# Kernel tuning notes

Measured on AMD Instinct MI355X. Metric: run time of the kernel, lower is better.

Reference implementation:

```python
import math
import jax, jax.numpy as jnp
import numpy as np
from jax import lax

B = 32; SEQ_LEN = 1024; PRED_LEN = 1024; ENC_IN = 7; MARK = 4; C_OUT = 7
D_MODEL = 128; D_INNER = 256; D_STATE = 16; D_CONV = 4; DT_RANK = 8; N_LAYER = 2


def setup_inputs() -> dict:
    key = jax.random.key(0)
    ks = jax.random.split(key, 16)
    f32 = jnp.float32
    inp = {}
    inp['x_enc'] = jax.random.normal(ks[0], (B, SEQ_LEN, ENC_IN), f32)
    inp['x_mark_enc'] = jax.random.uniform(ks[1], (B, SEQ_LEN, MARK), f32) - 0.5
    inp['x_dec'] = jax.random.normal(ks[2], (B, 512, ENC_IN), f32)
    inp['x_mark_dec'] = jax.random.uniform(ks[3], (B, 512, MARK), f32) - 0.5
    inp['token_W'] = jax.random.normal(ks[4], (D_MODEL, ENC_IN, 3), f32) * (1.0 / math.sqrt(3 * ENC_IN))
    inp['temporal_W'] = jax.random.normal(ks[5], (D_MODEL, MARK), f32) * 0.1
    inp['norm_w'] = jnp.ones((N_LAYER, D_MODEL), f32)
    inp['norm_b'] = jnp.zeros((N_LAYER, D_MODEL), f32)
    inp['in_proj_W'] = jax.random.normal(ks[6], (N_LAYER, 2 * D_INNER, D_MODEL), f32) * (1.0 / math.sqrt(D_MODEL))
    inp['conv_W'] = jax.random.normal(ks[7], (N_LAYER, D_INNER, D_CONV), f32) * 0.3
    inp['conv_b'] = jnp.zeros((N_LAYER, D_INNER), f32)
    inp['x_proj_W'] = jax.random.normal(ks[8], (N_LAYER, DT_RANK + 2 * D_STATE, D_INNER), f32) * (1.0 / math.sqrt(D_INNER))
    inp['dt_proj_W'] = jax.random.normal(ks[9], (N_LAYER, D_INNER, DT_RANK), f32) * (1.0 / math.sqrt(DT_RANK))
    inp['dt_proj_b'] = jax.random.normal(ks[10], (N_LAYER, D_INNER), f32) * 0.5 - 4.0  # softplus -> small dt, like mamba init
    inp['A_log'] = jnp.log(jnp.broadcast_to(jnp.arange(1, D_STATE + 1, dtype=f32), (N_LAYER, D_INNER, D_STATE)))
    inp['D_param'] = jnp.ones((N_LAYER, D_INNER), f32)
    inp['out_proj_W'] = jax.random.normal(ks[11], (N_LAYER, D_MODEL, D_INNER), f32) * (1.0 / math.sqrt(D_INNER))
    inp['normf_w'] = jnp.ones((D_MODEL,), f32)
    inp['normf_b'] = jnp.zeros((D_MODEL,), f32)
    inp['out_W'] = jax.random.normal(ks[12], (C_OUT, D_MODEL), f32) * (1.0 / math.sqrt(D_MODEL))
    return inp


def _layer_norm(x, w, b):
    mu = x.mean(-1, keepdims=True)
    var = ((x - mu) ** 2).mean(-1, keepdims=True)
    return (x - mu) * lax.rsqrt(var + 1e-5) * w + b


def _silu(x):
    return x * jax.nn.sigmoid(x)


def _pos_embedding(L, d):
    pos = jnp.arange(L, dtype=jnp.float32)[:, None]
    div = jnp.exp(jnp.arange(0, d, 2, dtype=jnp.float32) * (-math.log(10000.0) / d))
    pe = jnp.zeros((L, d), jnp.float32)
    pe = pe.at[:, 0::2].set(jnp.sin(pos * div))
    pe = pe.at[:, 1::2].set(jnp.cos(pos * div))
    return pe


def _embed(x_enc, x_mark_enc, token_W, temporal_W):
    # TokenEmbedding: Conv1d(enc_in->d_model, k=3, circular padding, no bias)
    xp = jnp.concatenate([x_enc[:, -1:], x_enc, x_enc[:, :1]], axis=1)  # circular pad by 1
    val = lax.conv_general_dilated(xp, token_W.transpose(2, 1, 0), (1,), 'VALID',
                                   dimension_numbers=('NWC', 'WIO', 'NWC'))
    temp = jnp.einsum('blf,df->bld', x_mark_enc, temporal_W)  # TimeFeatureEmbedding (no bias)
    return val + temp + _pos_embedding(x_enc.shape[1], D_MODEL)


def _mamba_mixer(x, in_W, cW, cb, xp_W, dtW, dtb, A_log_l, D_l, o_W):
    Bb, L, _ = x.shape
    xz = jnp.einsum('bld,ed->ble', x, in_W)  # [B,L,2*d_inner]
    xi, z = jnp.split(xz, 2, axis=-1)
    # causal depthwise conv1d (kernel d_conv)
    xpad = jnp.pad(xi, ((0, 0), (D_CONV - 1, 0), (0, 0)))
    kern = cW.T[:, None, :]  # [d_conv, 1, d_inner]
    u = lax.conv_general_dilated(xpad, kern, (1,), 'VALID', dimension_numbers=('NWC', 'WIO', 'NWC'),
                                 feature_group_count=D_INNER) + cb
    u = _silu(u)
    dbc = jnp.einsum('bld,ed->ble', u, xp_W)
    dt_r = dbc[..., :DT_RANK]
    Bm = dbc[..., DT_RANK:DT_RANK + D_STATE]
    Cm = dbc[..., DT_RANK + D_STATE:]
    dt = jax.nn.softplus(jnp.einsum('blr,dr->bld', dt_r, dtW) + dtb)  # [B,L,d_inner]
    A = -jnp.exp(A_log_l)  # [d_inner, d_state]

    def step(h, inp):
        dt_t, B_t, C_t, u_t = inp  # [B,d_inner], [B,d_state], [B,d_state], [B,d_inner]
        dA = jnp.exp(dt_t[..., None] * A)
        h = dA * h + dt_t[..., None] * B_t[:, None, :] * u_t[..., None]
        y = jnp.einsum('bds,bs->bd', h, C_t)
        return h, y

    h0 = jnp.zeros((Bb, D_INNER, D_STATE), x.dtype)
    _, ys = lax.scan(step, h0, (dt.transpose(1, 0, 2), Bm.transpose(1, 0, 2),
                                Cm.transpose(1, 0, 2), u.transpose(1, 0, 2)))
    y = ys.transpose(1, 0, 2) + u * D_l  # skip connection D*u
    y = y * _silu(z)
    return jnp.einsum('ble,de->bld', y, o_W)


def _mixer_model(x, norm_w, norm_b, in_proj_W, conv_W, conv_b, x_proj_W, dt_proj_W, dt_proj_b,
                 A_log, D_param, out_proj_W, normf_w, normf_b):
    hidden, residual = x, None
    for l in range(N_LAYER):
        residual = hidden if residual is None else hidden + residual
        hidden = _mamba_mixer(_layer_norm(residual, norm_w[l], norm_b[l]), in_proj_W[l], conv_W[l],
                              conv_b[l], x_proj_W[l], dt_proj_W[l], dt_proj_b[l], A_log[l],
                              D_param[l], out_proj_W[l])
    return _layer_norm(hidden + residual, normf_w, normf_b)


def reference(x_enc, x_mark_enc, x_dec, x_mark_dec, token_W, temporal_W, norm_w, norm_b,
              in_proj_W, conv_W, conv_b, x_proj_W, dt_proj_W, dt_proj_b, A_log, D_param,
              out_proj_W, normf_w, normf_b, out_W):
    h = _embed(x_enc, x_mark_enc, token_W, temporal_W)
    outs = []
    for _ in range((PRED_LEN - 1) // SEQ_LEN + 1):
        h = _mixer_model(h, norm_w, norm_b, in_proj_W, conv_W, conv_b, x_proj_W, dt_proj_W,
                         dt_proj_b, A_log, D_param, out_proj_W, normf_w, normf_b)
        outs.append(h)
    mamba_out = jnp.concatenate(outs, axis=1)[:, :PRED_LEN]
    return jnp.einsum('bld,cd->blc', mamba_out, out_W)
```

## Files before the change

### kernel.cpp

```cpp
#include <hip/hip_runtime.h>
#include <math.h>

#define B_  32
#define L_  1024
#define M_  (B_*L_)
#define DM  128
#define DI  256
#define DS  16
#define DC  4
#define DR  8
#define NL  2

__device__ __forceinline__ float silu_f(float x) { return x / (1.f + expf(-x)); }
__device__ __forceinline__ float softplus_f(float x) {
    return fmaxf(x, 0.f) + log1pf(expf(-fabsf(x)));
}

__global__ __launch_bounds__(256) void pe_kernel(float* __restrict__ pe) {
    int idx = blockIdx.x * 256 + threadIdx.x;
    int t = idx >> 6, i = idx & 63;
    float div = expf(-0.07195578415606394f * (float)(2 * i));
    float ang = (float)t * div;
    pe[t * 128 + 2 * i]     = sinf(ang);
    pe[t * 128 + 2 * i + 1] = cosf(ang);
}

__global__ __launch_bounds__(256) void embed_kernel(
        const float* __restrict__ x_enc, const float* __restrict__ x_mark,
        const float* __restrict__ tokW, const float* __restrict__ tempW,
        const float* __restrict__ pe, float* __restrict__ out) {
    int idx = blockIdx.x * 256 + threadIdx.x;
    int d = idx & 127;
    int m = idx >> 7;
    int b = m >> 10, t = m & 1023;
    const float* xb = x_enc + (size_t)b * L_ * 7;
    float acc = pe[t * 128 + d];
    #pragma unroll
    for (int w = 0; w < 3; ++w) {
        int tt = t + w - 1;
        tt = (tt < 0) ? (L_ - 1) : (tt >= L_ ? 0 : tt);
        const float* xr = xb + tt * 7;
        #pragma unroll
        for (int f = 0; f < 7; ++f) acc += xr[f] * tokW[(d * 7 + f) * 3 + w];
    }
    const float* mr = x_mark + (size_t)m * 4;
    #pragma unroll
    for (int f = 0; f < 4; ++f) acc += mr[f] * tempW[d * 4 + f];
    out[idx] = acc;
}

__global__ __launch_bounds__(256) void ln_kernel(
        const float* __restrict__ a, const float* __restrict__ b,
        const float* __restrict__ w, const float* __restrict__ bias,
        float* __restrict__ out_ln, float* __restrict__ out_res) {
    int wv = threadIdx.x >> 6, lane = threadIdx.x & 63;
    size_t m = (size_t)blockIdx.x * 4 + wv;
    size_t base = m * DM;
    float x0 = a[base + lane], x1 = a[base + lane + 64];
    if (b) { x0 += b[base + lane]; x1 += b[base + lane + 64]; }
    if (out_res) { out_res[base + lane] = x0; out_res[base + lane + 64] = x1; }
    float s = x0 + x1;
    #pragma unroll
    for (int o = 1; o < 64; o <<= 1) s += __shfl_xor(s, o, 64);
    float mu = s * (1.f / 128.f);
    float d0 = x0 - mu, d1 = x1 - mu;
    float v = d0 * d0 + d1 * d1;
    #pragma unroll
    for (int o = 1; o < 64; o <<= 1) v += __shfl_xor(v, o, 64);
    float inv = rsqrtf(v * (1.f / 128.f) + 1e-5f);
    out_ln[base + lane]      = d0 * inv * w[lane]      + bias[lane];
    out_ln[base + lane + 64] = d1 * inv * w[lane + 64] + bias[lane + 64];
}

__global__ __launch_bounds__(256) void gemm_inproj(
        const float* __restrict__ A, const float* __restrict__ W,
        float* __restrict__ xiT, float* __restrict__ zsilT) {
    __shared__ float As[32][128];
    __shared__ float Ws[32][128];
    int bm = blockIdx.y * 128, bn = blockIdx.x * 128;
    int tid = threadIdx.x, tx = tid & 15, ty = tid >> 4;
    float acc[8][8] = {};
    for (int k0 = 0; k0 < 128; k0 += 32) {
        #pragma unroll
        for (int i = 0; i < 4; ++i) {
            int idx = i * 256 + tid;
            int row = idx >> 3, c4 = (idx & 7) * 4;
            float4 a4 = *(const float4*)(A + (size_t)(bm + row) * 128 + k0 + c4);
            As[c4 + 0][row] = a4.x; As[c4 + 1][row] = a4.y;
            As[c4 + 2][row] = a4.z; As[c4 + 3][row] = a4.w;
            float4 w4 = *(const float4*)(W + (size_t)(bn + row) * 128 + k0 + c4);
            Ws[c4 + 0][row] = w4.x; Ws[c4 + 1][row] = w4.y;
            Ws[c4 + 2][row] = w4.z; Ws[c4 + 3][row] = w4.w;
        }
        __syncthreads();
        #pragma unroll
        for (int k = 0; k < 32; ++k) {
            float a[8], bb[8];
            *(float4*)&a[0]  = *(float4*)&As[k][ty * 8];
            *(float4*)&a[4]  = *(float4*)&As[k][ty * 8 + 4];
            *(float4*)&bb[0] = *(float4*)&Ws[k][tx * 8];
            *(float4*)&bb[4] = *(float4*)&Ws[k][tx * 8 + 4];
            #pragma unroll
            for (int i = 0; i < 8; ++i)
                #pragma unroll
                for (int j = 0; j < 8; ++j) acc[i][j] += a[i] * bb[j];
        }
        __syncthreads();
    }
    int b = bm >> 10, t0 = (bm & 1023) + ty * 8;
    if (bn < 256) {
        #pragma unroll
        for (int j = 0; j < 8; ++j) {
            int xd = bn + tx * 8 + j;
            float r[8];
            #pragma unroll
            for (int i = 0; i < 8; ++i) r[i] = acc[i][j];
            float* dst = xiT + ((size_t)(b * 256 + xd)) * 1024 + t0;
            *(float4*)dst       = *(float4*)&r[0];
            *(float4*)(dst + 4) = *(float4*)&r[4];
        }
    } else {
        #pragma unroll
        for (int j = 0; j < 8; ++j) {
            int zd = bn - 256 + tx * 8 + j;
            float r[8];
            #pragma unroll
            for (int i = 0; i < 8; ++i) r[i] = silu_f(acc[i][j]);
            float* dst = zsilT + ((size_t)(b * 256 + zd)) * 1024 + t0;
            *(float4*)dst       = *(float4*)&r[0];
            *(float4*)(dst + 4) = *(float4*)&r[4];
        }
    }
}

__global__ __launch_bounds__(256) void gemm_tn_128(
        const float* __restrict__ AT, const float* __restrict__ W,
        float* __restrict__ C, int M, int N, int K) {
    __shared__ float As[32][128];
    __shared__ float Ws[32][128];
    int bm = blockIdx.y * 128, bn = blockIdx.x * 128;
    int b = bm >> 10, tloc = bm & 1023;
    int tid = threadIdx.x, tx = tid & 15, ty = tid >> 4;
    float acc[8][8] = {};
    for (int k0 = 0; k0 < K; k0 += 32) {
        #pragma unroll
        for (int i = 0; i < 4; ++i) {
            int idx = i * 256 + tid;
            int k = idx >> 5, m4 = (idx & 31) * 4;
            float4 a4 = *(const float4*)(AT + ((size_t)b * K + k0 + k) * 1024 + tloc + m4);
            *(float4*)&As[k][m4] = a4;
            int row = idx >> 3, c4 = (idx & 7) * 4;
            float4 w4 = *(const float4*)(W + (size_t)(bn + row) * K + k0 + c4);
            Ws[c4 + 0][row] = w4.x; Ws[c4 + 1][row] = w4.y;
            Ws[c4 + 2][row] = w4.z; Ws[c4 + 3][row] = w4.w;
        }
        __syncthreads();
        #pragma unroll
        for (int k = 0; k < 32; ++k) {
            float a[8], bb[8];
            *(float4*)&a[0]  = *(float4*)&As[k][ty * 8];
            *(float4*)&a[4]  = *(float4*)&As[k][ty * 8 + 4];
            *(float4*)&bb[0] = *(float4*)&Ws[k][tx * 8];
            *(float4*)&bb[4] = *(float4*)&Ws[k][tx * 8 + 4];
            #pragma unroll
            for (int i = 0; i < 8; ++i)
                #pragma unroll
                for (int j = 0; j < 8; ++j) acc[i][j] += a[i] * bb[j];
        }
        __syncthreads();
    }
    #pragma unroll
    for (int i = 0; i < 8; ++i) {
        size_t row = (size_t)(bm + ty * 8 + i) * N + bn + tx * 8;
        *(float4*)(C + row)     = *(float4*)&acc[i][0];
        *(float4*)(C + row + 4) = *(float4*)&acc[i][4];
    }
}

__global__ __launch_bounds__(256) void gemm_tn_64(
        const float* __restrict__ AT, const float* __restrict__ W,
        float* __restrict__ C, int M, int N, int K) {
    __shared__ float As[16][68];
    __shared__ float Ws[16][68];
    int bm = blockIdx.y * 64, bn = blockIdx.x * 64;
    int b = bm >> 10, tloc = bm & 1023;
    int tid = threadIdx.x, tx = tid & 15, ty = tid >> 4;
    float acc[4][4] = {};
    for (int k0 = 0; k0 < K; k0 += 16) {
        {
            int k = tid >> 4, m4 = (tid & 15) * 4;
            float4 a4 = *(const float4*)(AT + ((size_t)b * K + k0 + k) * 1024 + tloc + m4);
            *(float4*)&As[k][m4] = a4;
        }
        #pragma unroll
        for (int i = 0; i < 4; ++i) {
            int r = i * 16 + ty;
            int n = bn + r;
            Ws[tx][r] = (n < N) ? W[(size_t)n * K + k0 + tx] : 0.f;
        }
        __syncthreads();
        #pragma unroll
        for (int k = 0; k < 16; ++k) {
            float a[4], bb[4];
            #pragma unroll
            for (int i = 0; i < 4; ++i) a[i] = As[k][ty * 4 + i];
            #pragma unroll
            for (int j = 0; j < 4; ++j) bb[j] = Ws[k][tx * 4 + j];
            #pragma unroll
            for (int i = 0; i < 4; ++i)
                #pragma unroll
                for (int j = 0; j < 4; ++j) acc[i][j] += a[i] * bb[j];
        }
        __syncthreads();
    }
    #pragma unroll
    for (int i = 0; i < 4; ++i) {
        int m = bm + ty * 4 + i;
        #pragma unroll
        for (int j = 0; j < 4; ++j) {
            int n = bn + tx * 4 + j;
            if (n < N) C[(size_t)m * N + n] = acc[i][j];
        }
    }
}

__global__ __launch_bounds__(256) void conv_T_kernel(
        const float* __restrict__ xiT, const float* __restrict__ cw,
        const float* __restrict__ cb, float* __restrict__ uT) {
    int wv = threadIdx.x >> 6, lane = threadIdx.x & 63;
    int rid = blockIdx.x * 4 + wv;
    int d = rid & 255;
    const float* src = xiT + (size_t)rid * 1024;
    int t0 = lane * 16;
    float x[20];
    {
        float4 p = (lane > 0) ? *(const float4*)(src + t0 - 4)
                              : make_float4(0.f, 0.f, 0.f, 0.f);
        *(float4*)&x[0] = p;
        #pragma unroll
        for (int c = 0; c < 4; ++c)
            *(float4*)&x[4 + c * 4] = *(const float4*)(src + t0 + c * 4);
    }
    float4 w4 = ((const float4*)cw)[d];
    float bias = cb[d];
    float* dst = uT + (size_t)rid * 1024 + t0;
    #pragma unroll
    for (int c = 0; c < 4; ++c) {
        float r[4];
        #pragma unroll
        for (int i = 0; i < 4; ++i) {
            int k = c * 4 + i;
            float acc = bias + x[k + 1] * w4.x + x[k + 2] * w4.y
                             + x[k + 3] * w4.z + x[k + 4] * w4.w;
            r[i] = silu_f(acc);
        }
        *(float4*)(dst + c * 4) = make_float4(r[0], r[1], r[2], r[3]);
    }
}

__global__ __launch_bounds__(256) void dbc_split_kernel(
        const float* __restrict__ dbc, const float* __restrict__ dtW,
        const float* __restrict__ dtb, float* __restrict__ dtT,
        float* __restrict__ BT, float* __restrict__ CT) {
    int m0 = blockIdx.x * 64;
    int b = m0 >> 10, t0 = m0 & 1023;
    {
        int n = threadIdx.x;
        float4 wa = ((const float4*)dtW)[n * 2];
        float4 wb = ((const float4*)dtW)[n * 2 + 1];
        float bias = dtb[n];
        float* dst = dtT + ((size_t)(b * 256 + n)) * 1024 + t0;
        for (int r4 = 0; r4 < 64; r4 += 4) {
            float o[4];
            #pragma unroll
            for (int i = 0; i < 4; ++i) {
                const float* row = dbc + (size_t)(m0 + r4 + i) * 40;
                float acc = bias + row[0] * wa.x + row[1] * wa.y + row[2] * wa.z + row[3] * wa.w
                                 + row[4] * wb.x + row[5] * wb.y + row[6] * wb.z + row[7] * wb.w;
                o[i] = softplus_f(acc);
            }
            *(float4*)(dst + r4) = make_float4(o[0], o[1], o[2], o[3]);
        }
    }
    {
        int s = threadIdx.x >> 3, q = threadIdx.x & 7;
        const float* src = dbc + (size_t)m0 * 40 + 8 + s;
        float* outp = ((s < 16) ? BT : CT) + ((size_t)(b * 16 + (s & 15))) * 1024 + t0 + q * 8;
        float v[8];
        #pragma unroll
        for (int i = 0; i < 8; ++i) v[i] = src[(size_t)(q * 8 + i) * 40];
        *(float4*)outp       = make_float4(v[0], v[1], v[2], v[3]);
        *(float4*)(outp + 4) = make_float4(v[4], v[5], v[6], v[7]);
    }
}

__global__ __launch_bounds__(256) void scan5_kernel(
        const float* __restrict__ dtT, const float* __restrict__ uT,
        const float* __restrict__ BT, const float* __restrict__ CT,
        const float* __restrict__ A_log, const float* __restrict__ zsilT,
        const float* __restrict__ Dp, float* __restrict__ yT) {
    int wv = threadIdx.x >> 6, lane = threadIdx.x & 63;
    int wid = blockIdx.x * 4 + wv;
    int b = wid >> 8, d = wid & 255;
    size_t base = (size_t)wid * 1024 + lane * 16;

    float dt[16], du[16], y[16], pcA[16], pcB[16];
    {
        const float4* p = (const float4*)(dtT + base);
        const float4* q = (const float4*)(uT + base);
        #pragma unroll
        for (int c = 0; c < 4; ++c) {
            float4 dv = p[c], uv = q[c];
            dt[c * 4 + 0] = dv.x; dt[c * 4 + 1] = dv.y; dt[c * 4 + 2] = dv.z; dt[c * 4 + 3] = dv.w;
            du[c * 4 + 0] = dv.x * uv.x; du[c * 4 + 1] = dv.y * uv.y;
            du[c * 4 + 2] = dv.z * uv.z; du[c * 4 + 3] = dv.w * uv.w;
        }
        #pragma unroll
        for (int i = 0; i < 16; ++i) y[i] = 0.f;
    }
    const float* Bb = BT + (size_t)b * 16 * 1024 + lane * 16;
    const float* Cb = CT + (size_t)b * 16 * 1024 + lane * 16;
    const float* Arow = A_log + d * 16;

    for (int p = 0; p < 8; ++p) {
        int s0 = 2 * p, s1 = 2 * p + 1;
        float4 B0[4], B1[4], C0[4], C1[4];
        #pragma unroll
        for (int c = 0; c < 4; ++c) {
            B0[c] = *(const float4*)(Bb + (size_t)s0 * 1024 + c * 4);
            B1[c] = *(const float4*)(Bb + (size_t)s1 * 1024 + c * 4);
            C0[c] = *(const float4*)(Cb + (size_t)s0 * 1024 + c * 4);
            C1[c] = *(const float4*)(Cb + (size_t)s1 * 1024 + c * 4);
        }
        float A2a = -expf(Arow[s0]) * 1.4426950408889634f;
        float A2b = -expf(Arow[s1]) * 1.4426950408889634f;
        float h0 = 0.f, P0 = 1.f, h1 = 0.f, P1 = 1.f;
        #pragma unroll
        for (int c = 0; c < 4; ++c) {
            float Bv0[4] = {B0[c].x, B0[c].y, B0[c].z, B0[c].w};
            float Cv0[4] = {C0[c].x, C0[c].y, C0[c].z, C0[c].w};
            float Bv1[4] = {B1[c].x, B1[c].y, B1[c].z, B1[c].w};
            float Cv1[4] = {C1[c].x, C1[c].y, C1[c].z, C1[c].w};
            #pragma unroll
            for (int i = 0; i < 4; ++i) {
                int ii = c * 4 + i;
                float a0 = __builtin_amdgcn_exp2f(dt[ii] * A2a);
                float a1 = __builtin_amdgcn_exp2f(dt[ii] * A2b);
                h0 = a0 * h0 + du[ii] * Bv0[i];  P0 *= a0;
                h1 = a1 * h1 + du[ii] * Bv1[i];  P1 *= a1;
                y[ii] += h0 * Cv0[i] + h1 * Cv1[i];
                pcA[ii] = P0 * Cv0[i];
                pcB[ii] = P1 * Cv1[i];
            }
        }
        float Aag0 = P0, E0 = h0, Aag1 = P1, E1 = h1;
        #pragma unroll
        for (int dlt = 1; dlt < 64; dlt <<= 1) {
            float Au0 = __shfl_up(Aag0, dlt, 64), Eu0 = __shfl_up(E0, dlt, 64);
            float Au1 = __shfl_up(Aag1, dlt, 64), Eu1 = __shfl_up(E1, dlt, 64);
            if (lane >= dlt) {
                E0 = Aag0 * Eu0 + E0;  Aag0 *= Au0;
                E1 = Aag1 * Eu1 + E1;  Aag1 *= Au1;
            }
        }
        float car0 = __shfl_up(E0, 1, 64), car1 = __shfl_up(E1, 1, 64);
        if (lane == 0) { car0 = 0.f; car1 = 0.f; }
        #pragma unroll
        for (int i = 0; i < 16; ++i) y[i] += car0 * pcA[i] + car1 * pcB[i];
    }

    float Dv = Dp[d];
    const float4* qz = (const float4*)(zsilT + base);
    float* dst = yT + base;
    #pragma unroll
    for (int c = 0; c < 4; ++c) {
        float4 zv = qz[c];
        float za[4] = {zv.x, zv.y, zv.z, zv.w};
        float r[4];
        #pragma unroll
        for (int i = 0; i < 4; ++i) {
            int ii = c * 4 + i;
            float u = (dt[ii] > 0.f) ? du[ii] * __builtin_amdgcn_rcpf(dt[ii]) : 0.f;
            r[i] = (y[ii] + u * Dv) * za[i];
        }
        *(float4*)(dst + c * 4) = make_float4(r[0], r[1], r[2], r[3]);
    }
}

__global__ __launch_bounds__(256) void outproj_kernel(
        const float* __restrict__ x, const float* __restrict__ W,
        float* __restrict__ out) {
    int wv = threadIdx.x >> 6, lane = threadIdx.x & 63;
    size_t m = (size_t)blockIdx.x * 4 + wv;
    float x0 = x[m * 128 + lane], x1 = x[m * 128 + lane + 64];
    #pragma unroll
    for (int c = 0; c < 7; ++c) {
        float p = x0 * W[c * 128 + lane] + x1 * W[c * 128 + lane + 64];
        #pragma unroll
        for (int o = 1; o < 64; o <<= 1) p += __shfl_xor(p, o, 64);
        if (lane == 0) out[m * 7 + c] = p;
    }
}

extern "C" void kernel_launch(void* const* d_in, const int* in_sizes, int n_in,
                              void* d_out, int out_size, void* d_ws, size_t ws_size,
                              hipStream_t stream) {
    const float* x_enc  = (const float*)d_in[0];
    const float* x_mark = (const float*)d_in[1];
    const float* tokW   = (const float*)d_in[4];
    const float* tempW  = (const float*)d_in[5];
    const float* norm_w = (const float*)d_in[6];
    const float* norm_b = (const float*)d_in[7];
    const float* inW    = (const float*)d_in[8];
    const float* convW  = (const float*)d_in[9];
    const float* convB  = (const float*)d_in[10];
    const float* xpW    = (const float*)d_in[11];
    const float* dtW    = (const float*)d_in[12];
    const float* dtbp   = (const float*)d_in[13];
    const float* A_log  = (const float*)d_in[14];
    const float* Dp     = (const float*)d_in[15];
    const float* outW   = (const float*)d_in[16];
    const float* nfw    = (const float*)d_in[17];
    const float* nfb    = (const float*)d_in[18];
    const float* finW   = (const float*)d_in[19];
    float* out = (float*)d_out;

    float* ws = (float*)d_ws;
    size_t o = 0;
    float* hidden   = ws + o; o += (size_t)M_ * DM;
    float* residual = ws + o; o += (size_t)M_ * DM;
    float* xln      = ws + o; o += (size_t)M_ * DM;
    float* xiT      = ws + o; o += (size_t)M_ * DI;
    float* zsilT    = ws + o; o += (size_t)M_ * DI;
    float* uT       = ws + o; o += (size_t)M_ * DI;
    float* dbc      = ws + o; o += (size_t)M_ * 40;
    float* dtT      = ws + o; o += (size_t)M_ * DI;
    float* yT       = ws + o; o += (size_t)M_ * DI;
    float* BT = xln;
    float* CT = xln + (size_t)B_ * DS * L_;
    float* pe = dbc;

    dim3 blk(256);
    pe_kernel<<<1024 * 64 / 256, blk, 0, stream>>>(pe);
    embed_kernel<<<M_ * DM / 256, blk, 0, stream>>>(x_enc, x_mark, tokW, tempW, pe, hidden);

    for (int l = 0; l < NL; ++l) {
        ln_kernel<<<M_ / 4, blk, 0, stream>>>(hidden, l ? residual : nullptr,
                                              norm_w + l * DM, norm_b + l * DM,
                                              xln, residual);
        gemm_inproj<<<dim3(4, M_ / 128), blk, 0, stream>>>(
            xln, inW + (size_t)l * 512 * DM, xiT, zsilT);
        conv_T_kernel<<<B_ * DI / 4, blk, 0, stream>>>(xiT, convW + l * DI * DC,
                                                       convB + l * DI, uT);
        gemm_tn_64<<<dim3(1, M_ / 64), blk, 0, stream>>>(
            uT, xpW + (size_t)l * 40 * DI, dbc, M_, 40, DI);
        dbc_split_kernel<<<M_ / 64, blk, 0, stream>>>(dbc, dtW + l * DI * DR,
                                                      dtbp + l * DI, dtT, BT, CT);
        scan5_kernel<<<B_ * DI / 4, blk, 0, stream>>>(dtT, uT, BT, CT,
                                                      A_log + l * DI * DS, zsilT,
                                                      Dp + l * DI, yT);
        gemm_tn_128<<<dim3(1, M_ / 128), blk, 0, stream>>>(
            yT, outW + (size_t)l * DM * DI, hidden, M_, DM, DI);
    }

    ln_kernel<<<M_ / 4, blk, 0, stream>>>(hidden, residual, nfw, nfb, xln, nullptr);
    outproj_kernel<<<M_ / 4, blk, 0, stream>>>(xln, finW, out);
}
```

Measured before the change: 696.5 us.

## Move projection GEMMs to split-bf16 MFMA with packed hi/lo activations

Replaces the three FP32 SIMT GEMMs (in_proj, x_proj, out_proj) with MFMA bf16 kernels that use a three-term hi/lo split (hi*hi + hi*lo + lo*hi) to keep roughly FP32 accuracy. The producers (layernorm, conv, scan) now emit activations as packed bf16 hi/lo pairs, and weights are converted once per call. The x_proj output is stored transposed so the separate dt/B/C split kernel becomes a smaller dt-only kernel, and scan reads B and C directly from it. This trades three MFMAs per tile, extra conversion work and some precision loss for tensor-core throughput on the GEMMs.

```diff
diff --git a/kernel.cpp b/kernel.cpp
--- a/kernel.cpp
+++ b/kernel.cpp
@@ -11,9 +11,38 @@
 #define DR  8
 #define NL  2
 
+typedef unsigned int  uint32;
+typedef unsigned short ush;
+typedef __attribute__((ext_vector_type(8))) short bf16x8;
+typedef __attribute__((ext_vector_type(4))) float f32x4;
+
 __device__ __forceinline__ float silu_f(float x) { return x / (1.f + expf(-x)); }
 __device__ __forceinline__ float softplus_f(float x) {
     return fmaxf(x, 0.f) + log1pf(expf(-fabsf(x)));
+}
+__device__ __forceinline__ ush f2bf(float x) {
+    union { float f; uint32 u; } v; v.f = x;
+    uint32 lsb = (v.u >> 16) & 1u;
+    v.u += 0x7fffu + lsb;
+    return (ush)(v.u >> 16);
+}
+__device__ __forceinline__ void split2(float x, ush& h, ush& l) {
+    h = f2bf(x);
+    float fh = __uint_as_float(((uint32)h) << 16);
+    l = f2bf(x - fh);
+}
+__device__ __forceinline__ uint32 pack_pair(float x) {
+    ush h, l; split2(x, h, l);
+    return (uint32)h | ((uint32)l << 16);
+}
+__device__ __forceinline__ float unpack_pair(uint32 v) {
+    return __uint_as_float(v << 16) + __uint_as_float(v & 0xffff0000u);
+}
+
+__global__ __launch_bounds__(256) void cvt_pair_kernel(
+        const float* __restrict__ src, ush* __restrict__ h, ush* __restrict__ l, int n) {
+    int i = blockIdx.x * 256 + threadIdx.x;
+    if (i < n) { ush hh, ll; split2(src[i], hh, ll); h[i] = hh; l[i] = ll; }
 }
 
 __global__ __launch_bounds__(256) void pe_kernel(float* __restrict__ pe) {
@@ -52,7 +81,8 @@
 __global__ __launch_bounds__(256) void ln_kernel(
         const float* __restrict__ a, const float* __restrict__ b,
         const float* __restrict__ w, const float* __restrict__ bias,
-        float* __restrict__ out_ln, float* __restrict__ out_res) {
+        float* __restrict__ out_f32, ush* __restrict__ outh, ush* __restrict__ outl,
+        float* __restrict__ out_res) {
     int wv = threadIdx.x >> 6, lane = threadIdx.x & 63;
     size_t m = (size_t)blockIdx.x * 4 + wv;
     size_t base = m * DM;
@@ -68,165 +98,162 @@
     #pragma unroll
     for (int o = 1; o < 64; o <<= 1) v += __shfl_xor(v, o, 64);
     float inv = rsqrtf(v * (1.f / 128.f) + 1e-5f);
-    out_ln[base + lane]      = d0 * inv * w[lane]      + bias[lane];
-    out_ln[base + lane + 64] = d1 * inv * w[lane + 64] + bias[lane + 64];
-}
-
-__global__ __launch_bounds__(256) void gemm_inproj(
-        const float* __restrict__ A, const float* __restrict__ W,
+    float r0 = d0 * inv * w[lane]      + bias[lane];
+    float r1 = d1 * inv * w[lane + 64] + bias[lane + 64];
+    if (out_f32) {
+        out_f32[base + lane] = r0; out_f32[base + lane + 64] = r1;
+    } else {
+        ush h, l;
+        split2(r0, h, l); outh[base + lane] = h;      outl[base + lane] = l;
+        split2(r1, h, l); outh[base + lane + 64] = h; outl[base + lane + 64] = l;
+    }
+}
+
+__global__ __launch_bounds__(256) void gemm_inproj_mfma(
+        const ush* __restrict__ Ah, const ush* __restrict__ Al,
+        const ush* __restrict__ Wh, const ush* __restrict__ Wl,
         float* __restrict__ xiT, float* __restrict__ zsilT) {
-    __shared__ float As[32][128];
-    __shared__ float Ws[32][128];
     int bm = blockIdx.y * 128, bn = blockIdx.x * 128;
-    int tid = threadIdx.x, tx = tid & 15, ty = tid >> 4;
-    float acc[8][8] = {};
+    int w = threadIdx.x >> 6, l = threadIdx.x & 63;
+    int lm = l & 15, lk8 = (l >> 4) * 8;
+    f32x4 acc[2][8];
+    #pragma unroll
+    for (int mi = 0; mi < 2; ++mi)
+        #pragma unroll
+        for (int ni = 0; ni < 8; ++ni) acc[mi][ni] = {0.f, 0.f, 0.f, 0.f};
+    const ush* ah = Ah + (size_t)(bm + w * 32 + lm) * 128;
+    const ush* al = Al + (size_t)(bm + w * 32 + lm) * 128;
+    const ush* wh = Wh + (size_t)(bn + lm) * 128;
+    const ush* wl = Wl + (size_t)(bn + lm) * 128;
     for (int k0 = 0; k0 < 128; k0 += 32) {
-        #pragma unroll
-        for (int i = 0; i < 4; ++i) {
-            int idx = i * 256 + tid;
-            int row = idx >> 3, c4 = (idx & 7) * 4;
-            float4 a4 = *(const float4*)(A + (size_t)(bm + row) * 128 + k0 + c4);
-            As[c4 + 0][row] = a4.x; As[c4 + 1][row] = a4.y;
-            As[c4 + 2][row] = a4.z; As[c4 + 3][row] = a4.w;
-            float4 w4 = *(const float4*)(W + (size_t)(bn + row) * 128 + k0 + c4);
-            Ws[c4 + 0][row] = w4.x; Ws[c4 + 1][row] = w4.y;
-            Ws[c4 + 2][row] = w4.z; Ws[c4 + 3][row] = w4.w;
-        }
+        bf16x8 aH[2], aL[2];
+        #pragma unroll
+        for (int mi = 0; mi < 2; ++mi) {
+            aH[mi] = *(const bf16x8*)(ah + mi * 16 * 128 + k0 + lk8);
+            aL[mi] = *(const bf16x8*)(al + mi * 16 * 128 + k0 + lk8);
+        }
+        #pragma unroll
+        for (int ni = 0; ni < 8; ++ni) {
+            bf16x8 wH = *(const bf16x8*)(wh + ni * 16 * 128 + k0 + lk8);
+            bf16x8 wLo = *(const bf16x8*)(wl + ni * 16 * 128 + k0 + lk8);
+            #pragma unroll
+            for (int mi = 0; mi < 2; ++mi) {
+                acc[mi][ni] = __builtin_amdgcn_mfma_f32_16x16x32_bf16(aL[mi], wH,  acc[mi][ni], 0, 0, 0);
+                acc[mi][ni] = __builtin_amdgcn_mfma_f32_16x16x32_bf16(aH[mi], wLo, acc[mi][ni], 0, 0, 0);
+                acc[mi][ni] = __builtin_amdgcn_mfma_f32_16x16x32_bf16(aH[mi], wH,  acc[mi][ni], 0, 0, 0);
+            }
+        }
+    }
+    int b = bm >> 10;
+    int tl0 = (bm & 1023) + w * 32 + (l >> 4) * 4;
+    #pragma unroll
+    for (int ni = 0; ni < 8; ++ni) {
+        int n = bn + ni * 16 + lm;
+        #pragma unroll
+        for (int mi = 0; mi < 2; ++mi) {
+            int tl = tl0 + mi * 16;
+            f32x4 v = acc[mi][ni];
+            if (bn < 256) {
+                *(f32x4*)(xiT + ((size_t)(b * 256 + n)) * 1024 + tl) = v;
+            } else {
+                f32x4 r;
+                #pragma unroll
+                for (int i = 0; i < 4; ++i) r[i] = silu_f(v[i]);
+                *(f32x4*)(zsilT + ((size_t)(b * 256 + n - 256)) * 1024 + tl) = r;
+            }
+        }
+    }
+}
+
+template<int NF, int KTOT>
+__global__ __launch_bounds__(256) void gemm_at_mfma(
+        const uint32* __restrict__ A32, const ush* __restrict__ Wh,
+        const ush* __restrict__ Wl, int Nvalid,
+        float* __restrict__ Cnm, float* __restrict__ Cmn) {
+    __shared__ uint32 As[128][68];
+    int bm = blockIdx.x * 128;
+    int b = bm >> 10, tloc = bm & 1023;
+    int tid = threadIdx.x;
+    int w = tid >> 6, l = tid & 63;
+    int lm = l & 15, lk8 = (l >> 4) * 8;
+    f32x4 acc[2][NF];
+    #pragma unroll
+    for (int mi = 0; mi < 2; ++mi)
+        #pragma unroll
+        for (int ni = 0; ni < NF; ++ni) acc[mi][ni] = {0.f, 0.f, 0.f, 0.f};
+
+    for (int k0 = 0; k0 < KTOT; k0 += 64) {
         __syncthreads();
-        #pragma unroll
-        for (int k = 0; k < 32; ++k) {
-            float a[8], bb[8];
-            *(float4*)&a[0]  = *(float4*)&As[k][ty * 8];
-            *(float4*)&a[4]  = *(float4*)&As[k][ty * 8 + 4];
-            *(float4*)&bb[0] = *(float4*)&Ws[k][tx * 8];
-            *(float4*)&bb[4] = *(float4*)&Ws[k][tx * 8 + 4];
+        {
+            int k = tid >> 2, mq = tid & 3;
+            const uint32* src = A32 + ((size_t)(b * KTOT + k0 + k)) * 1024 + tloc + mq * 32;
             #pragma unroll
-            for (int i = 0; i < 8; ++i)
+            for (int c = 0; c < 8; ++c) {
+                uint4 v = *(const uint4*)(src + c * 4);
+                As[mq * 32 + c * 4 + 0][k] = v.x;
+                As[mq * 32 + c * 4 + 1][k] = v.y;
+                As[mq * 32 + c * 4 + 2][k] = v.z;
+                As[mq * 32 + c * 4 + 3][k] = v.w;
+            }
+        }
+        __syncthreads();
+        #pragma unroll
+        for (int ks = 0; ks < 2; ++ks) {
+            int kk = ks * 32 + lk8;
+            bf16x8 aH[2], aL[2];
+            #pragma unroll
+            for (int mi = 0; mi < 2; ++mi) {
+                int m = w * 32 + mi * 16 + lm;
+                uint4 p0 = *(const uint4*)&As[m][kk];
+                uint4 p1 = *(const uint4*)&As[m][kk + 4];
+                uint32 u[8] = {p0.x, p0.y, p0.z, p0.w, p1.x, p1.y, p1.z, p1.w};
+                bf16x8 h, lo;
                 #pragma unroll
-                for (int j = 0; j < 8; ++j) acc[i][j] += a[i] * bb[j];
-        }
-        __syncthreads();
-    }
-    int b = bm >> 10, t0 = (bm & 1023) + ty * 8;
-    if (bn < 256) {
-        #pragma unroll
-        for (int j = 0; j < 8; ++j) {
-            int xd = bn + tx * 8 + j;
-            float r[8];
+                for (int j = 0; j < 8; ++j) {
+                    h[j]  = (short)(u[j] & 0xffffu);
+                    lo[j] = (short)(u[j] >> 16);
+                }
+                aH[mi] = h; aL[mi] = lo;
+            }
             #pragma unroll
-            for (int i = 0; i < 8; ++i) r[i] = acc[i][j];
-            float* dst = xiT + ((size_t)(b * 256 + xd)) * 1024 + t0;
-            *(float4*)dst       = *(float4*)&r[0];
-            *(float4*)(dst + 4) = *(float4*)&r[4];
-        }
-    } else {
-        #pragma unroll
-        for (int j = 0; j < 8; ++j) {
-            int zd = bn - 256 + tx * 8 + j;
-            float r[8];
-            #pragma unroll
-            for (int i = 0; i < 8; ++i) r[i] = silu_f(acc[i][j]);
-            float* dst = zsilT + ((size_t)(b * 256 + zd)) * 1024 + t0;
-            *(float4*)dst       = *(float4*)&r[0];
-            *(float4*)(dst + 4) = *(float4*)&r[4];
-        }
-    }
-}
-
-__global__ __launch_bounds__(256) void gemm_tn_128(
-        const float* __restrict__ AT, const float* __restrict__ W,
-        float* __restrict__ C, int M, int N, int K) {
-    __shared__ float As[32][128];
-    __shared__ float Ws[32][128];
-    int bm = blockIdx.y * 128, bn = blockIdx.x * 128;
-    int b = bm >> 10, tloc = bm & 1023;
-    int tid = threadIdx.x, tx = tid & 15, ty = tid >> 4;
-    float acc[8][8] = {};
-    for (int k0 = 0; k0 < K; k0 += 32) {
-        #pragma unroll
-        for (int i = 0; i < 4; ++i) {
-            int idx = i * 256 + tid;
-            int k = idx >> 5, m4 = (idx & 31) * 4;
-            float4 a4 = *(const float4*)(AT + ((size_t)b * K + k0 + k) * 1024 + tloc + m4);
-            *(float4*)&As[k][m4] = a4;
-            int row = idx >> 3, c4 = (idx & 7) * 4;
-            float4 w4 = *(const float4*)(W + (size_t)(bn + row) * K + k0 + c4);
-            Ws[c4 + 0][row] = w4.x; Ws[c4 + 1][row] = w4.y;
-            Ws[c4 + 2][row] = w4.z; Ws[c4 + 3][row] = w4.w;
-        }
-        __syncthreads();
-        #pragma unroll
-        for (int k = 0; k < 32; ++k) {
-            float a[8], bb[8];
-            *(float4*)&a[0]  = *(float4*)&As[k][ty * 8];
-            *(float4*)&a[4]  = *(float4*)&As[k][ty * 8 + 4];
-            *(float4*)&bb[0] = *(float4*)&Ws[k][tx * 8];
-            *(float4*)&bb[4] = *(float4*)&Ws[k][tx * 8 + 4];
-            #pragma unroll
-            for (int i = 0; i < 8; ++i)
+            for (int ni = 0; ni < NF; ++ni) {
+                int n = ni * 16 + lm;
+                bf16x8 wH = {0,0,0,0,0,0,0,0}, wLo = {0,0,0,0,0,0,0,0};
+                if (n < Nvalid) {
+                    wH  = *(const bf16x8*)(Wh + (size_t)n * KTOT + k0 + ks * 32 + lk8);
+                    wLo = *(const bf16x8*)(Wl + (size_t)n * KTOT + k0 + ks * 32 + lk8);
+                }
                 #pragma unroll
-                for (int j = 0; j < 8; ++j) acc[i][j] += a[i] * bb[j];
-        }
-        __syncthreads();
-    }
-    #pragma unroll
-    for (int i = 0; i < 8; ++i) {
-        size_t row = (size_t)(bm + ty * 8 + i) * N + bn + tx * 8;
-        *(float4*)(C + row)     = *(float4*)&acc[i][0];
-        *(float4*)(C + row + 4) = *(float4*)&acc[i][4];
-    }
-}
-
-__global__ __launch_bounds__(256) void gemm_tn_64(
-        const float* __restrict__ AT, const float* __restrict__ W,
-        float* __restrict__ C, int M, int N, int K) {
-    __shared__ float As[16][68];
-    __shared__ float Ws[16][68];
-    int bm = blockIdx.y * 64, bn = blockIdx.x * 64;
-    int b = bm >> 10, tloc = bm & 1023;
-    int tid = threadIdx.x, tx = tid & 15, ty = tid >> 4;
-    float acc[4][4] = {};
-    for (int k0 = 0; k0 < K; k0 += 16) {
-        {
-            int k = tid >> 4, m4 = (tid & 15) * 4;
-            float4 a4 = *(const float4*)(AT + ((size_t)b * K + k0 + k) * 1024 + tloc + m4);
-            *(float4*)&As[k][m4] = a4;
-        }
-        #pragma unroll
-        for (int i = 0; i < 4; ++i) {
-            int r = i * 16 + ty;
-            int n = bn + r;
-            Ws[tx][r] = (n < N) ? W[(size_t)n * K + k0 + tx] : 0.f;
-        }
-        __syncthreads();
-        #pragma unroll
-        for (int k = 0; k < 16; ++k) {
-            float a[4], bb[4];
-            #pragma unroll
-            for (int i = 0; i < 4; ++i) a[i] = As[k][ty * 4 + i];
-            #pragma unroll
-            for (int j = 0; j < 4; ++j) bb[j] = Ws[k][tx * 4 + j];
-            #pragma unroll
-            for (int i = 0; i < 4; ++i)
+                for (int mi = 0; mi < 2; ++mi) {
+                    acc[mi][ni] = __builtin_amdgcn_mfma_f32_16x16x32_bf16(aL[mi], wH,  acc[mi][ni], 0, 0, 0);
+                    acc[mi][ni] = __builtin_amdgcn_mfma_f32_16x16x32_bf16(aH[mi], wLo, acc[mi][ni], 0, 0, 0);
+                    acc[mi][ni] = __builtin_amdgcn_mfma_f32_16x16x32_bf16(aH[mi], wH,  acc[mi][ni], 0, 0, 0);
+                }
+            }
+        }
+    }
+    int m0 = w * 32 + (l >> 4) * 4;
+    #pragma unroll
+    for (int ni = 0; ni < NF; ++ni) {
+        int n = ni * 16 + lm;
+        #pragma unroll
+        for (int mi = 0; mi < 2; ++mi) {
+            f32x4 v = acc[mi][ni];
+            int mg = bm + m0 + mi * 16;
+            if (Cnm) {
+                if (n < Nvalid) *(f32x4*)(Cnm + (size_t)n * M_ + mg) = v;
+            } else {
                 #pragma unroll
-                for (int j = 0; j < 4; ++j) acc[i][j] += a[i] * bb[j];
-        }
-        __syncthreads();
-    }
-    #pragma unroll
-    for (int i = 0; i < 4; ++i) {
-        int m = bm + ty * 4 + i;
-        #pragma unroll
-        for (int j = 0; j < 4; ++j) {
-            int n = bn + tx * 4 + j;
-            if (n < N) C[(size_t)m * N + n] = acc[i][j];
+                for (int r = 0; r < 4; ++r)
+                    Cmn[(size_t)(mg + r) * Nvalid + n] = v[r];
+            }
         }
     }
 }
 
 __global__ __launch_bounds__(256) void conv_T_kernel(
         const float* __restrict__ xiT, const float* __restrict__ cw,
-        const float* __restrict__ cb, float* __restrict__ uT) {
+        const float* __restrict__ cb, uint32* __restrict__ uT32) {
     int wv = threadIdx.x >> 6, lane = threadIdx.x & 63;
     int rid = blockIdx.x * 4 + wv;
     int d = rid & 255;
@@ -243,62 +270,56 @@
     }
     float4 w4 = ((const float4*)cw)[d];
     float bias = cb[d];
-    float* dst = uT + (size_t)rid * 1024 + t0;
+    uint32* dst = uT32 + (size_t)rid * 1024 + t0;
     #pragma unroll
     for (int c = 0; c < 4; ++c) {
-        float r[4];
+        uint4 o;
+        uint32 ov[4];
         #pragma unroll
         for (int i = 0; i < 4; ++i) {
             int k = c * 4 + i;
             float acc = bias + x[k + 1] * w4.x + x[k + 2] * w4.y
                              + x[k + 3] * w4.z + x[k + 4] * w4.w;
-            r[i] = silu_f(acc);
-        }
-        *(float4*)(dst + c * 4) = make_float4(r[0], r[1], r[2], r[3]);
-    }
-}
-
-__global__ __launch_bounds__(256) void dbc_split_kernel(
-        const float* __restrict__ dbc, const float* __restrict__ dtW,
-        const float* __restrict__ dtb, float* __restrict__ dtT,
-        float* __restrict__ BT, float* __restrict__ CT) {
+            ov[i] = pack_pair(silu_f(acc));
+        }
+        o.x = ov[0]; o.y = ov[1]; o.z = ov[2]; o.w = ov[3];
+        *(uint4*)(dst + c * 4) = o;
+    }
+}
+
+__global__ __launch_bounds__(256) void dtT_kernel(
+        const float* __restrict__ dbcT, const float* __restrict__ dtW,
+        const float* __restrict__ dtb, float* __restrict__ dtT) {
+    int n = threadIdx.x;
     int m0 = blockIdx.x * 64;
     int b = m0 >> 10, t0 = m0 & 1023;
-    {
-        int n = threadIdx.x;
-        float4 wa = ((const float4*)dtW)[n * 2];
-        float4 wb = ((const float4*)dtW)[n * 2 + 1];
-        float bias = dtb[n];
-        float* dst = dtT + ((size_t)(b * 256 + n)) * 1024 + t0;
-        for (int r4 = 0; r4 < 64; r4 += 4) {
-            float o[4];
+    float wk[8];
+    *(float4*)&wk[0] = ((const float4*)dtW)[n * 2];
+    *(float4*)&wk[4] = ((const float4*)dtW)[n * 2 + 1];
+    float bias = dtb[n];
+    float* dst = dtT + ((size_t)(b * 256 + n)) * 1024 + t0;
+    for (int r4 = 0; r4 < 64; r4 += 4) {
+        float col[8][4];
+        #pragma unroll
+        for (int k = 0; k < 8; ++k)
+            *(float4*)col[k] = *(const float4*)(dbcT + (size_t)k * M_ + m0 + r4);
+        float o[4];
+        #pragma unroll
+        for (int i = 0; i < 4; ++i) {
+            float a = bias;
             #pragma unroll
-            for (int i = 0; i < 4; ++i) {
-                const float* row = dbc + (size_t)(m0 + r4 + i) * 40;
-                float acc = bias + row[0] * wa.x + row[1] * wa.y + row[2] * wa.z + row[3] * wa.w
-                                 + row[4] * wb.x + row[5] * wb.y + row[6] * wb.z + row[7] * wb.w;
-                o[i] = softplus_f(acc);
-            }
-            *(float4*)(dst + r4) = make_float4(o[0], o[1], o[2], o[3]);
-        }
-    }
-    {
-        int s = threadIdx.x >> 3, q = threadIdx.x & 7;
-        const float* src = dbc + (size_t)m0 * 40 + 8 + s;
-        float* outp = ((s < 16) ? BT : CT) + ((size_t)(b * 16 + (s & 15))) * 1024 + t0 + q * 8;
-        float v[8];
-        #pragma unroll
-        for (int i = 0; i < 8; ++i) v[i] = src[(size_t)(q * 8 + i) * 40];
-        *(float4*)outp       = make_float4(v[0], v[1], v[2], v[3]);
-        *(float4*)(outp + 4) = make_float4(v[4], v[5], v[6], v[7]);
+            for (int k = 0; k < 8; ++k) a += col[k][i] * wk[k];
+            o[i] = softplus_f(a);
+        }
+        *(float4*)(dst + r4) = make_float4(o[0], o[1], o[2], o[3]);
     }
 }
 
 __global__ __launch_bounds__(256) void scan5_kernel(
-        const float* __restrict__ dtT, const float* __restrict__ uT,
-        const float* __restrict__ BT, const float* __restrict__ CT,
-        const float* __restrict__ A_log, const float* __restrict__ zsilT,
-        const float* __restrict__ Dp, float* __restrict__ yT) {
+        const float* __restrict__ dtT, const uint32* __restrict__ uT32,
+        const float* __restrict__ dbcT, const float* __restrict__ A_log,
+        const float* __restrict__ zsilT, const float* __restrict__ Dp,
+        uint32* __restrict__ yT32) {
     int wv = threadIdx.x >> 6, lane = threadIdx.x & 63;
     int wid = blockIdx.x * 4 + wv;
     int b = wid >> 8, d = wid & 255;
@@ -307,19 +328,21 @@
     float dt[16], du[16], y[16], pcA[16], pcB[16];
     {
         const float4* p = (const float4*)(dtT + base);
-        const float4* q = (const float4*)(uT + base);
+        const uint4*  q = (const uint4*)(uT32 + base);
         #pragma unroll
         for (int c = 0; c < 4; ++c) {
-            float4 dv = p[c], uv = q[c];
+            float4 dv = p[c]; uint4 uv = q[c];
             dt[c * 4 + 0] = dv.x; dt[c * 4 + 1] = dv.y; dt[c * 4 + 2] = dv.z; dt[c * 4 + 3] = dv.w;
-            du[c * 4 + 0] = dv.x * uv.x; du[c * 4 + 1] = dv.y * uv.y;
-            du[c * 4 + 2] = dv.z * uv.z; du[c * 4 + 3] = dv.w * uv.w;
+            du[c * 4 + 0] = dv.x * unpack_pair(uv.x);
+            du[c * 4 + 1] = dv.y * unpack_pair(uv.y);
+            du[c * 4 + 2] = dv.z * unpack_pair(uv.z);
+            du[c * 4 + 3] = dv.w * unpack_pair(uv.w);
         }
         #pragma unroll
         for (int i = 0; i < 16; ++i) y[i] = 0.f;
     }
-    const float* Bb = BT + (size_t)b * 16 * 1024 + lane * 16;
-    const float* Cb = CT + (size_t)b * 16 * 1024 + lane * 16;
+    const float* Bb = dbcT + (size_t)8  * M_ + (size_t)b * 1024 + lane * 16;
+    const float* Cb = dbcT + (size_t)24 * M_ + (size_t)b * 1024 + lane * 16;
     const float* Arow = A_log + d * 16;
 
     for (int p = 0; p < 8; ++p) {
@@ -327,10 +350,10 @@
         float4 B0[4], B1[4], C0[4], C1[4];
         #pragma unroll
         for (int c = 0; c < 4; ++c) {
-            B0[c] = *(const float4*)(Bb + (size_t)s0 * 1024 + c * 4);
-            B1[c] = *(const float4*)(Bb + (size_t)s1 * 1024 + c * 4);
-            C0[c] = *(const float4*)(Cb + (size_t)s0 * 1024 + c * 4);
-            C1[c] = *(const float4*)(Cb + (size_t)s1 * 1024 + c * 4);
+            B0[c] = *(const float4*)(Bb + (size_t)s0 * M_ + c * 4);
+            B1[c] = *(const float4*)(Bb + (size_t)s1 * M_ + c * 4);
+            C0[c] = *(const float4*)(Cb + (size_t)s0 * M_ + c * 4);
+            C1[c] = *(const float4*)(Cb + (size_t)s1 * M_ + c * 4);
         }
         float A2a = -expf(Arow[s0]) * 1.4426950408889634f;
         float A2b = -expf(Arow[s1]) * 1.4426950408889634f;
@@ -371,19 +394,20 @@
 
     float Dv = Dp[d];
     const float4* qz = (const float4*)(zsilT + base);
-    float* dst = yT + base;
+    uint32* dst = yT32 + base;
     #pragma unroll
     for (int c = 0; c < 4; ++c) {
         float4 zv = qz[c];
         float za[4] = {zv.x, zv.y, zv.z, zv.w};
-        float r[4];
+        uint32 ov[4];
         #pragma unroll
         for (int i = 0; i < 4; ++i) {
             int ii = c * 4 + i;
             float u = (dt[ii] > 0.f) ? du[ii] * __builtin_amdgcn_rcpf(dt[ii]) : 0.f;
-            r[i] = (y[ii] + u * Dv) * za[i];
-        }
-        *(float4*)(dst + c * 4) = make_float4(r[0], r[1], r[2], r[3]);
+            ov[i] = pack_pair((y[ii] + u * Dv) * za[i]);
+        }
+        uint4 o; o.x = ov[0]; o.y = ov[1]; o.z = ov[2]; o.w = ov[3];
+        *(uint4*)(dst + c * 4) = o;
     }
 }
 
@@ -427,42 +451,58 @@
 
     float* ws = (float*)d_ws;
     size_t o = 0;
-    float* hidden   = ws + o; o += (size_t)M_ * DM;
-    float* residual = ws + o; o += (size_t)M_ * DM;
-    float* xln      = ws + o; o += (size_t)M_ * DM;
-    float* xiT      = ws + o; o += (size_t)M_ * DI;
-    float* zsilT    = ws + o; o += (size_t)M_ * DI;
-    float* uT       = ws + o; o += (size_t)M_ * DI;
-    float* dbc      = ws + o; o += (size_t)M_ * 40;
-    float* dtT      = ws + o; o += (size_t)M_ * DI;
-    float* yT       = ws + o; o += (size_t)M_ * DI;
-    float* BT = xln;
-    float* CT = xln + (size_t)B_ * DS * L_;
-    float* pe = dbc;
+    float*  hidden   = ws + o; o += (size_t)M_ * DM;
+    float*  residual = ws + o; o += (size_t)M_ * DM;
+    float*  xlnF     = ws + o; o += (size_t)M_ * DM;
+    float*  xiT      = ws + o; o += (size_t)M_ * DI;
+    float*  zsilT    = ws + o; o += (size_t)M_ * DI;
+    uint32* uT32     = (uint32*)(ws + o); o += (size_t)M_ * DI;
+    float*  dbcT     = ws + o; o += (size_t)M_ * 40;
+    float*  dtT      = ws + o; o += (size_t)M_ * DI;
+    uint32* yT32     = (uint32*)(ws + o); o += (size_t)M_ * DI;
+    ush* inWh  = (ush*)(ws + o); o += (size_t)NL * 512 * DM / 2;
+    ush* inWl  = (ush*)(ws + o); o += (size_t)NL * 512 * DM / 2;
+    ush* xpWh  = (ush*)(ws + o); o += (size_t)NL * 40 * DI / 2;
+    ush* xpWl  = (ush*)(ws + o); o += (size_t)NL * 40 * DI / 2;
+    ush* outWh = (ush*)(ws + o); o += (size_t)NL * DM * DI / 2;
+    ush* outWl = (ush*)(ws + o); o += (size_t)NL * DM * DI / 2;
+    ush* xlnh = (ush*)xlnF;
+    ush* xlnl = xlnh + (size_t)M_ * DM;
+    float* pe = dbcT;
 
     dim3 blk(256);
     pe_kernel<<<1024 * 64 / 256, blk, 0, stream>>>(pe);
     embed_kernel<<<M_ * DM / 256, blk, 0, stream>>>(x_enc, x_mark, tokW, tempW, pe, hidden);
+    {
+        int n1 = NL * 512 * DM, n2 = NL * 40 * DI, n3 = NL * DM * DI;
+        cvt_pair_kernel<<<(n1 + 255) / 256, blk, 0, stream>>>(inW,  inWh,  inWl,  n1);
+        cvt_pair_kernel<<<(n2 + 255) / 256, blk, 0, stream>>>(xpW,  xpWh,  xpWl,  n2);
+        cvt_pair_kernel<<<(n3 + 255) / 256, blk, 0, stream>>>(outW, outWh, outWl, n3);
+    }
 
     for (int l = 0; l < NL; ++l) {
         ln_kernel<<<M_ / 4, blk, 0, stream>>>(hidden, l ? residual : nullptr,
                                               norm_w + l * DM, norm_b + l * DM,
-                                              xln, residual);
-        gemm_inproj<<<dim3(4, M_ / 128), blk, 0, stream>>>(
-            xln, inW + (size_t)l * 512 * DM, xiT, zsilT);
+                                              nullptr, xlnh, xlnl, residual);
+        gemm_inproj_mfma<<<dim3(4, M_ / 128), blk, 0, stream>>>(
+            xlnh, xlnl, inWh + (size_t)l * 512 * DM, inWl + (size_t)l * 512 * DM,
+            xiT, zsilT);
         conv_T_kernel<<<B_ * DI / 4, blk, 0, stream>>>(xiT, convW + l * DI * DC,
-                                                       convB + l * DI, uT);
-        gemm_tn_64<<<dim3(1, M_ / 64), blk, 0, stream>>>(
-            uT, xpW + (size_t)l * 40 * DI, dbc, M_, 40, DI);
-        dbc_split_kernel<<<M_ / 64, blk, 0, stream>>>(dbc, dtW + l * DI * DR,
-                                                      dtbp + l * DI, dtT, BT, CT);
-        scan5_kernel<<<B_ * DI / 4, blk, 0, stream>>>(dtT, uT, BT, CT,
+                                                       convB + l * DI, uT32);
+        gemm_at_mfma<3, 256><<<M_ / 128, blk, 0, stream>>>(
+            uT32, xpWh + (size_t)l * 40 * DI, xpWl + (size_t)l * 40 * DI,
+            40, dbcT, nullptr);
+        dtT_kernel<<<M_ / 64, blk, 0, stream>>>(dbcT, dtW + l * DI * DR,
+                                                dtbp + l * DI, dtT);
+        scan5_kernel<<<B_ * DI / 4, blk, 0, stream>>>(dtT, uT32, dbcT,
                                                       A_log + l * DI * DS, zsilT,
-                                                      Dp + l * DI, yT);
-        gemm_tn_128<<<dim3(1, M_ / 128), blk, 0, stream>>>(
-            yT, outW + (size_t)l * DM * DI, hidden, M_, DM, DI);
-    }
-
-    ln_kernel<<<M_ / 4, blk, 0, stream>>>(hidden, residual, nfw, nfb, xln, nullptr);
-    outproj_kernel<<<M_ / 4, blk, 0, stream>>>(xln, finW, out);
-}
+                                                      Dp + l * DI, yT32);
+        gemm_at_mfma<8, 256><<<M_ / 128, blk, 0, stream>>>(
+            yT32, outWh + (size_t)l * DM * DI, outWl + (size_t)l * DM * DI,
+            128, nullptr, hidden);
+    }
+
+    ln_kernel<<<M_ / 4, blk, 0, stream>>>(hidden, residual, nfw, nfb,
+                                          xlnF, nullptr, nullptr, nullptr);
+    outproj_kernel<<<M_ / 4, blk, 0, stream>>>(xlnF, finW, out);
+}
```

Result: faster. 629.4 us (-9.6%).
